# Performance work log

Hardware: AMD Instinct MI355X
Metric: run time of the kernel (lower is better)

The kernel has to match this reference:

```python
import jax, jax.numpy as jnp
import numpy as np

T, B, E, H = 128, 1024, 1024, 1024  # batch must equal hidden (original code uses Whh @ h)


def setup_inputs() -> dict:
    key = jax.random.key(0)
    ks = jax.random.split(key, 10)
    s = 1.0 / np.sqrt(H).astype(np.float32)  # ~xavier scale, avoids gate saturation
    inp = {
        'X': jax.random.normal(ks[0], (T, B, E), dtype=jnp.float32),
        'Wii': jax.random.normal(ks[1], (E, H), dtype=jnp.float32) * s,
        'Whi': jax.random.normal(ks[2], (H, H), dtype=jnp.float32) * s,
        'bi': jnp.zeros((H,), dtype=jnp.float32),
        'Wif': jax.random.normal(ks[3], (E, H), dtype=jnp.float32) * s,
        'Whf': jax.random.normal(ks[4], (H, H), dtype=jnp.float32) * s,
        'bf': jnp.zeros((H,), dtype=jnp.float32),
        'Wig': jax.random.normal(ks[5], (E, H), dtype=jnp.float32) * s,
        'Whg': jax.random.normal(ks[6], (H, H), dtype=jnp.float32) * s,
        'bg': jnp.zeros((H,), dtype=jnp.float32),
        'Wio': jax.random.normal(ks[7], (E, H), dtype=jnp.float32) * s,
        'Who': jax.random.normal(ks[8], (H, H), dtype=jnp.float32) * s,
        'bo': jnp.zeros((H,), dtype=jnp.float32),
    }
    return inp


def reference(X, Wii, Whi, bi, Wif, Whf, bf, Wig, Whg, bg, Wio, Who, bo):
    # Faithful to the original: recurrent term is Whh @ h (NOT h @ Whh),
    # which requires batch == hidden as in the source module.
    batch = X.shape[1]
    hid = Wii.shape[1]
    h0 = jnp.zeros((batch, hid), dtype=X.dtype)
    c0 = jnp.zeros((batch, hid), dtype=X.dtype)

    def step(carry, x_t):
        h, c = carry
        i = jax.nn.sigmoid(x_t @ Wii + Whi @ h + bi)
        f = jax.nn.sigmoid(x_t @ Wif + Whf @ h + bf)
        g = jnp.tanh(x_t @ Wig + Whg @ h + bg)
        o = jax.nn.sigmoid(x_t @ Wio + Who @ h + bo)
        c_new = f * c + i * g
        h_new = o * jnp.tanh(c_new)
        return (h_new, c_new), h_new

    (h_t, c_t), hidden_sequence = jax.lax.scan(step, (h0, c0), X)
    return hidden_sequence, (h_t, c_t)
```

## Files before the change

### kernel.cpp

```cpp
#include <hip/hip_runtime.h>
#include <cstdint>

typedef __attribute__((ext_vector_type(8))) short bf16x8;
typedef __attribute__((ext_vector_type(4))) float f32x4;
typedef __attribute__((ext_vector_type(4))) unsigned int u32x4;

#define AS1 __attribute__((address_space(1)))
#define AS3 __attribute__((address_space(3)))

__device__ __forceinline__ unsigned short f2bf(float f) {
  unsigned int u = __builtin_bit_cast(unsigned int, f);
  return (unsigned short)((u + 0x7fffu + ((u >> 16) & 1u)) >> 16);
}
__device__ __forceinline__ float bf2f(unsigned short h) {
  unsigned int u = ((unsigned int)h) << 16;
  return __builtin_bit_cast(float, u);
}
__device__ __forceinline__ float sigm(float x) { return 1.f / (1.f + __expf(-x)); }
__device__ __forceinline__ float tanh_f(float x) {
  float e = __expf(2.f * x);
  return 1.f - 2.f / (e + 1.f);
}
__device__ __forceinline__ void gload16(const void* g, void* l) {
  __builtin_amdgcn_global_load_lds((const AS1 unsigned int*)g, (AS3 unsigned int*)l, 16, 0, 0);
}
__device__ __forceinline__ int swz(int e) { return e ^ (((e >> 6) & 7) << 3); }


__global__ __launch_bounds__(256) void conv_wh_kernel(
    const float4* __restrict__ w0, const float4* __restrict__ w1,
    const float4* __restrict__ w2, const float4* __restrict__ w3,
    unsigned long long* __restrict__ dst) {
  int i = blockIdx.x * 256 + threadIdx.x;
  int g = i >> 18;
  const float4* s = g == 0 ? w0 : g == 1 ? w1 : g == 2 ? w2 : w3;
  float4 v = s[i & 0x3FFFF];
  unsigned long long p = (unsigned long long)f2bf(v.x) |
                         ((unsigned long long)f2bf(v.y) << 16) |
                         ((unsigned long long)f2bf(v.z) << 32) |
                         ((unsigned long long)f2bf(v.w) << 48);
  dst[i] = p;
}

__global__ __launch_bounds__(256) void conv_wiT_kernel(
    const float* __restrict__ w0, const float* __restrict__ w1,
    const float* __restrict__ w2, const float* __restrict__ w3,
    unsigned short* __restrict__ dst) {
  __shared__ unsigned short ls[64][72];
  int bid = blockIdx.x;
  int g = bid >> 8;
  int t2 = bid & 255;
  int tj = t2 & 15, tk = t2 >> 4;
  const float* W = g == 0 ? w0 : g == 1 ? w1 : g == 2 ? w2 : w3;
  int k0 = tk * 64, j0 = tj * 64;
  int ty = threadIdx.x >> 6, tx = threadIdx.x & 63;
#pragma unroll
  for (int r = 0; r < 16; ++r) {
    int k = k0 + ty * 16 + r;
    ls[tx][ty * 16 + r] = f2bf(W[k * 1024 + j0 + tx]);
  }
  __syncthreads();
#pragma unroll
  for (int r = 0; r < 16; ++r) {
    int jl = ty * 16 + r;
    dst[(size_t)(g * 1024 + j0 + jl) * 1024 + k0 + tx] = ls[jl][tx];
  }
}

__global__ __launch_bounds__(256) void conv_bias_kernel(
    const float* __restrict__ b0, const float* __restrict__ b1,
    const float* __restrict__ b2, const float* __restrict__ b3,
    float* __restrict__ dst) {
  int i = blockIdx.x * 256 + threadIdx.x;
  const float* s = (i >> 10) == 0 ? b0 : (i >> 10) == 1 ? b1 : (i >> 10) == 2 ? b2 : b3;
  dst[i] = s[i & 1023];
}

__global__ __launch_bounds__(256) void conv_x_kernel(
    const float4* __restrict__ src, unsigned long long* __restrict__ dst, int n4) {
  int i = blockIdx.x * 256 + threadIdx.x;
  if (i < n4) {
    float4 v = src[i];
    dst[i] = (unsigned long long)f2bf(v.x) |
             ((unsigned long long)f2bf(v.y) << 16) |
             ((unsigned long long)f2bf(v.z) << 32) |
             ((unsigned long long)f2bf(v.w) << 48);
  }
}

__global__ __launch_bounds__(512, 2) void xproj_gemm_kernel(
    const unsigned short* __restrict__ A,
    const unsigned short* __restrict__ Bt,
    unsigned short* __restrict__ C,
    int Mc) {
  __shared__ __align__(16) unsigned short smem[2][2][256 * 64];
  int xcd = blockIdx.x & 7;
  int i5 = blockIdx.x >> 3;
  int bn = xcd * 2 + (i5 & 1);
  int bm = i5 >> 1;
  int m0 = bm * 256, n0 = bn * 256;
  int tid = threadIdx.x, w = tid >> 6, lane = tid & 63;
  int wm = w >> 2, wn = w & 3;
  int l15 = lane & 15, l4 = lane >> 4;

  f32x4 acc[8][4];
#pragma unroll
  for (int i = 0; i < 8; ++i)
#pragma unroll
    for (int j = 0; j < 4; ++j) acc[i][j] = (f32x4)0.f;

  auto stage = [&](int buf, int kt) {
    int kk = kt * 64;
#pragma unroll
    for (int u = 0; u < 4; ++u) {
      int cid = u * 512 + tid;
      int r = cid >> 3, s = cid & 7;
      int sk = kk + ((s ^ (r & 7)) << 3);
      gload16(&A[(size_t)(m0 + r) * 1024 + sk],
              &smem[buf][0][(u * 512 + w * 64) * 8]);
    }
#pragma unroll
    for (int u = 0; u < 4; ++u) {
      int cid = u * 512 + tid;
      int r = cid >> 3, s = cid & 7;
      int sk = kk + ((s ^ (r & 7)) << 3);
      gload16(&Bt[(size_t)(n0 + r) * 1024 + sk],
              &smem[buf][1][(u * 512 + w * 64) * 8]);
    }
  };

  stage(0, 0);
  asm volatile("s_waitcnt vmcnt(0)" ::: "memory");
  __builtin_amdgcn_sched_barrier(0);
  __builtin_amdgcn_s_barrier();
  __builtin_amdgcn_sched_barrier(0);

  int cur = 0;
  for (int t = 0; t < 16; ++t) {
    if (t < 15) stage(cur ^ 1, t + 1);
#pragma unroll
    for (int kss = 0; kss < 2; ++kss) {
      bf16x8 af[8], bfr[4];
#pragma unroll
      for (int mf = 0; mf < 8; ++mf) {
        int e = (wm * 128 + mf * 16 + l15) * 64 + kss * 32 + l4 * 8;
        af[mf] = *(const bf16x8*)&smem[cur][0][swz(e)];
      }
#pragma unroll
      for (int nf = 0; nf < 4; ++nf) {
        int e = (wn * 64 + nf * 16 + l15) * 64 + kss * 32 + l4 * 8;
        bfr[nf] = *(const bf16x8*)&smem[cur][1][swz(e)];
      }
      __builtin_amdgcn_s_setprio(1);
#pragma unroll
      for (int mf = 0; mf < 8; ++mf)
#pragma unroll
        for (int nf = 0; nf < 4; ++nf)
          acc[mf][nf] = __builtin_amdgcn_mfma_f32_16x16x32_bf16(
              af[mf], bfr[nf], acc[mf][nf], 0, 0, 0);
      __builtin_amdgcn_s_setprio(0);
    }
    asm volatile("s_waitcnt vmcnt(0)" ::: "memory");
    __builtin_amdgcn_sched_barrier(0);
    __builtin_amdgcn_s_barrier();
    __builtin_amdgcn_sched_barrier(0);
    cur ^= 1;
  }

  unsigned short* lsC = &smem[0][0][0];
#pragma unroll
  for (int h = 0; h < 2; ++h) {
    __syncthreads();
    if ((wn >> 1) == h) {
#pragma unroll
      for (int mf = 0; mf < 8; ++mf)
#pragma unroll
        for (int nf = 0; nf < 4; ++nf)
#pragma unroll
          for (int r = 0; r < 4; ++r) {
            int row = wm * 128 + mf * 16 + l4 * 4 + r;
            int col = (wn & 1) * 64 + nf * 16 + l15;
            lsC[row * 136 + col] = f2bf(acc[mf][nf][r]);
          }
    }
    __syncthreads();
#pragma unroll
    for (int u = 0; u < 8; ++u) {
      int chunk = u * 512 + tid;
      int row = chunk >> 4, c8 = chunk & 15;
      u32x4 v = *(const u32x4*)&lsC[row * 136 + c8 * 8];
      __builtin_nontemporal_store(
          v, (u32x4*)&C[(size_t)(m0 + row) * 4096 + n0 + h * 128 + c8 * 8]);
    }
  }
}

__global__ __launch_bounds__(256) void lstm_step_kernel(
    const unsigned short* __restrict__ Wh,
    const unsigned short* __restrict__ hT,
    const unsigned short* __restrict__ Xp,
    const float* __restrict__ bias,
    float* __restrict__ cst,
    float* __restrict__ out_h,
    float* __restrict__ out_ht,
    float* __restrict__ out_ct,
    unsigned short* __restrict__ hT_next,
    int isLast) {
  __shared__ unsigned short lsA[3][128 * 64];
  __shared__ unsigned short lsB[3][64 * 64];
  int bx = blockIdx.x;
  int xcd = bx & 7, idx = bx >> 3;
  int bb = xcd * 4 + (idx & 3);
  int bj = idx >> 2;
  int b0 = bb * 32, j0 = bj * 64;
  int tid = threadIdx.x, w = tid >> 6, lane = tid & 63;
  int wm = w >> 1, wn = w & 1;
  int l15 = lane & 15, l4 = lane >> 4;
  int bbase = b0 + wm * 16 + l4 * 4;

  float bias_pre[4][2];
  float c_pre[2][4];
  unsigned short xp_pre[4][2][4];
#pragma unroll
  for (int n = 0; n < 2; ++n) {
    int j = j0 + wn * 32 + n * 16 + l15;
#pragma unroll
    for (int g = 0; g < 4; ++g) bias_pre[g][n] = bias[g * 1024 + j];
#pragma unroll
    for (int r = 0; r < 4; ++r) {
      c_pre[n][r] = cst[(size_t)(bbase + r) * 1024 + j];
#pragma unroll
      for (int g = 0; g < 4; ++g)
        xp_pre[g][n][r] = Xp[(size_t)(bbase + r) * 4096 + g * 1024 + j];
    }
  }

  f32x4 acc[4][2];
#pragma unroll
  for (int g = 0; g < 4; ++g)
#pragma unroll
    for (int n = 0; n < 2; ++n) acc[g][n] = (f32x4)0.f;

  auto stage = [&](int buf, int kk) {
#pragma unroll
    for (int ld = 0; ld < 4; ++ld) {
      int cid = ld * 256 + tid;
      int r = cid >> 3, kc = (cid & 7) * 8;
      int sk = kk + (kc ^ ((r & 7) << 3));
      int grow = ((r >> 4) & 3) * 1024 + b0 + (r >> 6) * 16 + (r & 15);
      gload16(&Wh[(size_t)grow * 1024 + sk], &lsA[buf][(ld * 256 + w * 64) * 8]);
    }
#pragma unroll
    for (int u = 0; u < 2; ++u) {
      int cid = u * 256 + tid;
      int r = cid >> 3, kc = (cid & 7) * 8;
      int sk = kk + (kc ^ ((r & 7) << 3));
      gload16(&hT[(size_t)(j0 + r) * 1024 + sk], &lsB[buf][(u * 256 + w * 64) * 8]);
    }
  };
  auto compute = [&](int buf) {
    bf16x8 af[4][2], bfr[2][2];
#pragma unroll
    for (int g = 0; g < 4; ++g)
#pragma unroll
      for (int kss = 0; kss < 2; ++kss) {
        int e = (wm * 64 + g * 16 + l15) * 64 + kss * 32 + l4 * 8;
        af[g][kss] = *(const bf16x8*)&lsA[buf][swz(e)];
      }
#pragma unroll
    for (int n = 0; n < 2; ++n)
#pragma unroll
      for (int kss = 0; kss < 2; ++kss) {
        int e = (wn * 32 + n * 16 + l15) * 64 + kss * 32 + l4 * 8;
        bfr[n][kss] = *(const bf16x8*)&lsB[buf][swz(e)];
      }
    __builtin_amdgcn_s_setprio(1);
#pragma unroll
    for (int g = 0; g < 4; ++g)
#pragma unroll
      for (int n = 0; n < 2; ++n)
#pragma unroll
        for (int kss = 0; kss < 2; ++kss)
          acc[g][n] = __builtin_amdgcn_mfma_f32_16x16x32_bf16(
              af[g][kss], bfr[n][kss], acc[g][n], 0, 0, 0);
    __builtin_amdgcn_s_setprio(0);
  };

  stage(0, 0);
  stage(1, 64);
#pragma unroll
  for (int it = 0; it < 16; ++it) {
    if (it < 15) asm volatile("s_waitcnt vmcnt(6)" ::: "memory");
    else         asm volatile("s_waitcnt vmcnt(0)" ::: "memory");
    __builtin_amdgcn_sched_barrier(0);
    __builtin_amdgcn_s_barrier();
    __builtin_amdgcn_sched_barrier(0);
    if (it + 2 < 16) stage((it + 2) % 3, (it + 2) * 64);
    compute(it % 3);
    asm volatile("s_waitcnt lgkmcnt(0)" ::: "memory");
    __builtin_amdgcn_sched_barrier(0);
  }

#pragma unroll
  for (int n = 0; n < 2; ++n) {
    int j = j0 + wn * 32 + n * 16 + l15;
    float hn[4], cn[4];
#pragma unroll
    for (int r = 0; r < 4; ++r) {
      int b = bbase + r;
      float pi = acc[0][n][r] + bf2f(xp_pre[0][n][r]) + bias_pre[0][n];
      float pf = acc[1][n][r] + bf2f(xp_pre[1][n][r]) + bias_pre[1][n];
      float pg = acc[2][n][r] + bf2f(xp_pre[2][n][r]) + bias_pre[2][n];
      float po = acc[3][n][r] + bf2f(xp_pre[3][n][r]) + bias_pre[3][n];
      float ig = sigm(pi), fg = sigm(pf), gg = tanh_f(pg), og = sigm(po);
      float c_new = fg * c_pre[n][r] + ig * gg;
      cst[(size_t)b * 1024 + j] = c_new;
      cn[r] = c_new;
      hn[r] = og * tanh_f(c_new);
      __builtin_nontemporal_store(hn[r], &out_h[(size_t)b * 1024 + j]);
    }
    unsigned long long hp = (unsigned long long)f2bf(hn[0]) |
                            ((unsigned long long)f2bf(hn[1]) << 16) |
                            ((unsigned long long)f2bf(hn[2]) << 32) |
                            ((unsigned long long)f2bf(hn[3]) << 48);
    *(unsigned long long*)&hT_next[(size_t)j * 1024 + bbase] = hp;
    if (isLast) {
#pragma unroll
      for (int r = 0; r < 4; ++r) {
        int b = bbase + r;
        __builtin_nontemporal_store(hn[r], &out_ht[(size_t)b * 1024 + j]);
        __builtin_nontemporal_store(cn[r], &out_ct[(size_t)b * 1024 + j]);
      }
    }
  }
}

extern "C" void kernel_launch(void* const* d_in, const int* in_sizes, int n_in,
                              void* d_out, int out_size, void* d_ws, size_t ws_size,
                              hipStream_t stream) {
  const float* X   = (const float*)d_in[0];
  const float* Wii = (const float*)d_in[1];
  const float* Whi = (const float*)d_in[2];
  const float* bi  = (const float*)d_in[3];
  const float* Wif = (const float*)d_in[4];
  const float* Whf = (const float*)d_in[5];
  const float* bfv = (const float*)d_in[6];
  const float* Wig = (const float*)d_in[7];
  const float* Whg = (const float*)d_in[8];
  const float* bg  = (const float*)d_in[9];
  const float* Wio = (const float*)d_in[10];
  const float* Who = (const float*)d_in[11];
  const float* bo  = (const float*)d_in[12];
  float* out = (float*)d_out;

  char* wsp = (char*)d_ws;
  size_t off = 0;
  auto walloc = [&](size_t b) -> void* {
    void* p = wsp + off;
    off += (b + 255) & ~(size_t)255;
    return p;
  };
  unsigned short* WiT = (unsigned short*)walloc(4096ull * 1024 * 2);
  unsigned short* Wh  = (unsigned short*)walloc(4096ull * 1024 * 2);
  float* bias = (float*)walloc(4096 * 4);
  unsigned short* hT0 = (unsigned short*)walloc(1024ull * 1024 * 2);
  unsigned short* hT1 = (unsigned short*)walloc(1024ull * 1024 * 2);
  float* cbuf = (float*)walloc(1024ull * 1024 * 4);
  size_t fixed = off;

  long long avail = (long long)ws_size - (long long)fixed - (1ll << 20);
  int Tc = (int)(avail / (10ll << 20));
  if (Tc < 1) Tc = 1;
  if (Tc > 128) Tc = 128;
  unsigned short* Xbf = (unsigned short*)walloc((size_t)Tc * 1024 * 1024 * 2);
  unsigned short* Xp  = (unsigned short*)walloc((size_t)Tc * 1024 * 4096 * 2);

  conv_wh_kernel<<<4096, 256, 0, stream>>>((const float4*)Whi, (const float4*)Whf,
                                           (const float4*)Whg, (const float4*)Who,
                                           (unsigned long long*)Wh);
  conv_wiT_kernel<<<1024, 256, 0, stream>>>(Wii, Wif, Wig, Wio, WiT);
  conv_bias_kernel<<<16, 256, 0, stream>>>(bi, bfv, bg, bo, bias);
  hipMemsetAsync(hT0, 0, 1024ull * 1024 * 2, stream);
  hipMemsetAsync(cbuf, 0, 1024ull * 1024 * 4, stream);

  for (int t0 = 0; t0 < 128; t0 += Tc) {
    int tc = (128 - t0 < Tc) ? (128 - t0) : Tc;
    int n4 = tc * 262144;
    conv_x_kernel<<<n4 / 256, 256, 0, stream>>>(
        (const float4*)(X + (size_t)t0 * 1048576),
        (unsigned long long*)Xbf, n4);
    xproj_gemm_kernel<<<tc * 64, 512, 0, stream>>>(Xbf, WiT, Xp, tc * 1024);
    for (int i = 0; i < tc; ++i) {
      int t = t0 + i;
      lstm_step_kernel<<<512, 256, 0, stream>>>(
          Wh, (t & 1) ? hT1 : hT0,
          Xp + (size_t)i * 1024 * 4096,
          bias, cbuf,
          out + (size_t)t * 1048576,
          out + 134217728ull,
          out + 135266304ull,
          (t & 1) ? hT0 : hT1,
          (t == 127) ? 1 : 0);
    }
  }
}
```

Before: 3.432 ms.

## Pipeline xproj GEMM in quarter-tile phases with interleaved staging and MFMA

```diff
diff --git a/kernel.cpp b/kernel.cpp
--- a/kernel.cpp
+++ b/kernel.cpp
@@ -88,7 +88,7 @@
   }
 }
 
-__global__ __launch_bounds__(512, 2) void xproj_gemm_kernel(
+__global__ __launch_bounds__(512) void xproj_gemm_kernel(
     const unsigned short* __restrict__ A,
     const unsigned short* __restrict__ Bt,
     unsigned short* __restrict__ C,
@@ -109,80 +109,156 @@
 #pragma unroll
     for (int j = 0; j < 4; ++j) acc[i][j] = (f32x4)0.f;
 
-  auto stage = [&](int buf, int kt) {
+  auto stageHalf = [&](int buf, int kt, int X) {
     int kk = kt * 64;
-#pragma unroll
-    for (int u = 0; u < 4; ++u) {
+    unsigned short* dst = &smem[buf][X & 1][0];
+    const unsigned short* src = (X & 1) ? Bt : A;
+    int gbase = (X & 1) ? n0 : m0;
+    int r0 = (X >> 1) * 128;
+#pragma unroll
+    for (int u = 0; u < 2; ++u) {
       int cid = u * 512 + tid;
-      int r = cid >> 3, s = cid & 7;
-      int sk = kk + ((s ^ (r & 7)) << 3);
-      gload16(&A[(size_t)(m0 + r) * 1024 + sk],
-              &smem[buf][0][(u * 512 + w * 64) * 8]);
-    }
-#pragma unroll
-    for (int u = 0; u < 4; ++u) {
-      int cid = u * 512 + tid;
-      int r = cid >> 3, s = cid & 7;
-      int sk = kk + ((s ^ (r & 7)) << 3);
-      gload16(&Bt[(size_t)(n0 + r) * 1024 + sk],
-              &smem[buf][1][(u * 512 + w * 64) * 8]);
-    }
-  };
-
-  stage(0, 0);
-  asm volatile("s_waitcnt vmcnt(0)" ::: "memory");
-  __builtin_amdgcn_sched_barrier(0);
-  __builtin_amdgcn_s_barrier();
-  __builtin_amdgcn_sched_barrier(0);
-
-  int cur = 0;
+      int rl = r0 + (cid >> 3), s = cid & 7;
+      int sk = kk + ((s ^ (rl & 7)) << 3);
+      gload16(&src[(size_t)(gbase + rl) * 1024 + sk],
+              &dst[r0 * 64 + (u * 512 + w * 64) * 8]);
+    }
+  };
+  auto rdA = [&](int buf, int lo, bf16x8 (&arr)[4][2]) {
+#pragma unroll
+    for (int mf = 0; mf < 4; ++mf)
+#pragma unroll
+      for (int kss = 0; kss < 2; ++kss) {
+        int row = lo * 128 + wm * 64 + mf * 16 + l15;
+        arr[mf][kss] =
+            *(const bf16x8*)&smem[buf][0][swz(row * 64 + kss * 32 + l4 * 8)];
+      }
+  };
+  auto rdB = [&](int buf, int lo, bf16x8 (&arr)[2][2]) {
+#pragma unroll
+    for (int nf = 0; nf < 2; ++nf)
+#pragma unroll
+      for (int kss = 0; kss < 2; ++kss) {
+        int row = lo * 128 + wn * 32 + nf * 16 + l15;
+        arr[nf][kss] =
+            *(const bf16x8*)&smem[buf][1][swz(row * 64 + kss * 32 + l4 * 8)];
+      }
+  };
+
+  bf16x8 af03[4][2], af47[4][2], bfr01[2][2], bfr23[2][2];
+
+  stageHalf(0, 0, 0); stageHalf(0, 0, 1); stageHalf(0, 0, 2); stageHalf(0, 0, 3);
+
   for (int t = 0; t < 16; ++t) {
-    if (t < 15) stage(cur ^ 1, t + 1);
-#pragma unroll
-    for (int kss = 0; kss < 2; ++kss) {
-      bf16x8 af[8], bfr[4];
-#pragma unroll
-      for (int mf = 0; mf < 8; ++mf) {
-        int e = (wm * 128 + mf * 16 + l15) * 64 + kss * 32 + l4 * 8;
-        af[mf] = *(const bf16x8*)&smem[cur][0][swz(e)];
-      }
-#pragma unroll
-      for (int nf = 0; nf < 4; ++nf) {
-        int e = (wn * 64 + nf * 16 + l15) * 64 + kss * 32 + l4 * 8;
-        bfr[nf] = *(const bf16x8*)&smem[cur][1][swz(e)];
-      }
+    int c = t & 1;
+    if (t < 15) asm volatile("s_waitcnt vmcnt(6)" ::: "memory");
+    else        asm volatile("s_waitcnt vmcnt(6)" ::: "memory");
+    __builtin_amdgcn_sched_barrier(0);
+    __builtin_amdgcn_s_barrier();
+    __builtin_amdgcn_sched_barrier(0);
+    rdA(c, 0, af03);
+    if (t + 1 < 16) stageHalf(c ^ 1, t + 1, 0);
+    asm volatile("s_waitcnt lgkmcnt(0)" ::: "memory");
+    __builtin_amdgcn_sched_barrier(0);
+    if (t > 0) {
       __builtin_amdgcn_s_setprio(1);
 #pragma unroll
-      for (int mf = 0; mf < 8; ++mf)
-#pragma unroll
-        for (int nf = 0; nf < 4; ++nf)
+      for (int mf = 0; mf < 4; ++mf)
+#pragma unroll
+        for (int nf = 0; nf < 2; ++nf)
+#pragma unroll
+          for (int kss = 0; kss < 2; ++kss)
+            acc[4 + mf][2 + nf] = __builtin_amdgcn_mfma_f32_16x16x32_bf16(
+                af47[mf][kss], bfr23[nf][kss], acc[4 + mf][2 + nf], 0, 0, 0);
+      __builtin_amdgcn_s_setprio(0);
+    }
+    if (t < 15) asm volatile("s_waitcnt vmcnt(6)" ::: "memory");
+    else        asm volatile("s_waitcnt vmcnt(4)" ::: "memory");
+    __builtin_amdgcn_sched_barrier(0);
+    __builtin_amdgcn_s_barrier();
+    __builtin_amdgcn_sched_barrier(0);
+    rdB(c, 0, bfr01);
+    if (t + 1 < 16) stageHalf(c ^ 1, t + 1, 1);
+    asm volatile("s_waitcnt lgkmcnt(0)" ::: "memory");
+    __builtin_amdgcn_sched_barrier(0);
+    __builtin_amdgcn_s_setprio(1);
+#pragma unroll
+    for (int mf = 0; mf < 4; ++mf)
+#pragma unroll
+      for (int nf = 0; nf < 2; ++nf)
+#pragma unroll
+        for (int kss = 0; kss < 2; ++kss)
           acc[mf][nf] = __builtin_amdgcn_mfma_f32_16x16x32_bf16(
-              af[mf], bfr[nf], acc[mf][nf], 0, 0, 0);
-      __builtin_amdgcn_s_setprio(0);
-    }
-    asm volatile("s_waitcnt vmcnt(0)" ::: "memory");
+              af03[mf][kss], bfr01[nf][kss], acc[mf][nf], 0, 0, 0);
+    __builtin_amdgcn_s_setprio(0);
+    if (t < 15) asm volatile("s_waitcnt vmcnt(6)" ::: "memory");
+    else        asm volatile("s_waitcnt vmcnt(2)" ::: "memory");
     __builtin_amdgcn_sched_barrier(0);
     __builtin_amdgcn_s_barrier();
     __builtin_amdgcn_sched_barrier(0);
-    cur ^= 1;
+    rdA(c, 1, af47);
+    if (t + 1 < 16) stageHalf(c ^ 1, t + 1, 2);
+    asm volatile("s_waitcnt lgkmcnt(0)" ::: "memory");
+    __builtin_amdgcn_sched_barrier(0);
+    __builtin_amdgcn_s_setprio(1);
+#pragma unroll
+    for (int mf = 0; mf < 4; ++mf)
+#pragma unroll
+      for (int nf = 0; nf < 2; ++nf)
+#pragma unroll
+        for (int kss = 0; kss < 2; ++kss)
+          acc[4 + mf][nf] = __builtin_amdgcn_mfma_f32_16x16x32_bf16(
+              af47[mf][kss], bfr01[nf][kss], acc[4 + mf][nf], 0, 0, 0);
+    __builtin_amdgcn_s_setprio(0);
+    if (t < 15) asm volatile("s_waitcnt vmcnt(6)" ::: "memory");
+    else        asm volatile("s_waitcnt vmcnt(0)" ::: "memory");
+    __builtin_amdgcn_sched_barrier(0);
+    __builtin_amdgcn_s_barrier();
+    __builtin_amdgcn_sched_barrier(0);
+    rdB(c, 1, bfr23);
+    if (t + 1 < 16) stageHalf(c ^ 1, t + 1, 3);
+    asm volatile("s_waitcnt lgkmcnt(0)" ::: "memory");
+    __builtin_amdgcn_sched_barrier(0);
+    __builtin_amdgcn_s_setprio(1);
+#pragma unroll
+    for (int mf = 0; mf < 4; ++mf)
+#pragma unroll
+      for (int nf = 0; nf < 2; ++nf)
+#pragma unroll
+        for (int kss = 0; kss < 2; ++kss)
+          acc[mf][2 + nf] = __builtin_amdgcn_mfma_f32_16x16x32_bf16(
+              af03[mf][kss], bfr23[nf][kss], acc[mf][2 + nf], 0, 0, 0);
+    __builtin_amdgcn_s_setprio(0);
+  }
+  {
+    __builtin_amdgcn_s_setprio(1);
+#pragma unroll
+    for (int mf = 0; mf < 4; ++mf)
+#pragma unroll
+      for (int nf = 0; nf < 2; ++nf)
+#pragma unroll
+        for (int kss = 0; kss < 2; ++kss)
+          acc[4 + mf][2 + nf] = __builtin_amdgcn_mfma_f32_16x16x32_bf16(
+              af47[mf][kss], bfr23[nf][kss], acc[4 + mf][2 + nf], 0, 0, 0);
+    __builtin_amdgcn_s_setprio(0);
   }
 
   unsigned short* lsC = &smem[0][0][0];
 #pragma unroll
   for (int h = 0; h < 2; ++h) {
     __syncthreads();
-    if ((wn >> 1) == h) {
-#pragma unroll
-      for (int mf = 0; mf < 8; ++mf)
-#pragma unroll
-        for (int nf = 0; nf < 4; ++nf)
-#pragma unroll
-          for (int r = 0; r < 4; ++r) {
-            int row = wm * 128 + mf * 16 + l4 * 4 + r;
-            int col = (wn & 1) * 64 + nf * 16 + l15;
-            lsC[row * 136 + col] = f2bf(acc[mf][nf][r]);
-          }
-    }
+#pragma unroll
+    for (int mf = 0; mf < 8; ++mf)
+#pragma unroll
+      for (int f = 0; f < 2; ++f) {
+        int nf = h * 2 + f;
+        int rowl = (mf < 4 ? wm * 64 + mf * 16 : 128 + wm * 64 + (mf - 4) * 16)
+                   + l4 * 4;
+        int coll = wn * 32 + f * 16 + l15;
+#pragma unroll
+        for (int r = 0; r < 4; ++r)
+          lsC[(rowl + r) * 136 + coll] = f2bf(acc[mf][nf][r]);
+      }
     __syncthreads();
 #pragma unroll
     for (int u = 0; u < 8; ++u) {
```

Result: faster. 3.362 ms (-2.0%).
